# Kernel tuning notes

Measured on AMD Instinct MI355X. Metric: run time of the kernel, lower is better.

Reference implementation:

```python
import jax, jax.numpy as jnp
import numpy as np
import math

B, T, D = 1, 2048, 2048
H, HD = 16, 128          # n_head, head_dim = D // H
L = 512                  # latent_dims
RD = 64                  # rope_dims
K = 32                   # top-k selected tokens per query
THETA = 10000.0


def rope_tables(rd, t_max):
    freqs = 1.0 / (THETA ** (jnp.arange(0, rd, 2, dtype=jnp.float32) / rd))
    t = jnp.arange(t_max, dtype=jnp.float32)
    ang = jnp.outer(t, freqs)                      # (T, rd/2)
    cos = jnp.concatenate([jnp.cos(ang), jnp.cos(ang)], axis=-1)  # (T, rd)
    sin = jnp.concatenate([jnp.sin(ang), jnp.sin(ang)], axis=-1)
    return cos, sin


def rotate_half(x):
    d = x.shape[-1] // 2
    return jnp.concatenate([-x[..., d:], x[..., :d]], axis=-1)


def apply_rope(x, cos, sin):
    # x: (B, H, T, rd); cos/sin: (T, rd) -> broadcast over B, H
    t = x.shape[2]
    return x * cos[None, None, :t] + rotate_half(x) * sin[None, None, :t]


def setup_inputs() -> dict:
    key = jax.random.key(0)
    ks = jax.random.split(key, 10)
    s = lambda fan_in: 1.0 / math.sqrt(fan_in)
    inp = {
        'x': jax.random.normal(ks[0], (B, T, D), dtype=jnp.float32),
        'Wqd': jax.random.normal(ks[1], (D, L), dtype=jnp.float32) * s(D),
        'Wqu': jax.random.normal(ks[2], (L, D), dtype=jnp.float32) * s(L),
        'Wqr': jax.random.normal(ks[3], (L, H * RD), dtype=jnp.float32) * s(L),
        'Wkvd': jax.random.normal(ks[4], (D, L), dtype=jnp.float32) * s(D),
        'Wku': jax.random.normal(ks[5], (L, D), dtype=jnp.float32) * s(L),
        'Wvu': jax.random.normal(ks[6], (L, D), dtype=jnp.float32) * s(L),
        'Wkr': jax.random.normal(ks[7], (D, RD), dtype=jnp.float32) * s(D),
        'Wo': jax.random.normal(ks[8], (D, D), dtype=jnp.float32) * s(D),
        'topk_idx': jax.random.randint(ks[9], (B, T, K), 0, T, dtype=jnp.int64)
            if jax.config.jax_enable_x64 else
            jax.random.randint(ks[9], (B, T, K), 0, T, dtype=jnp.int32),
    }
    return inp


def reference(x, Wqd, Wqu, Wqr, Wkvd, Wku, Wvu, Wkr, Wo, topk_idx):
    cos, sin = rope_tables(RD, T)

    ql = x @ Wqd                                               # (B,T,L)
    q = (ql @ Wqu).reshape(B, T, H, HD).transpose(0, 2, 1, 3)  # (B,H,T,hd)
    qr = (ql @ Wqr).reshape(B, T, H, RD).transpose(0, 2, 1, 3)
    qr = apply_rope(qr, cos, sin)                              # (B,H,T,rd)

    ckv = x @ Wkvd                                             # (B,T,L)
    k = (ckv @ Wku).reshape(B, T, H, HD).transpose(0, 2, 1, 3) # (B,H,T,hd)
    v = (ckv @ Wvu).reshape(B, T, H, HD).transpose(0, 2, 1, 3)
    kr = apply_rope((x @ Wkr)[:, None], cos, sin)[:, 0]        # (B,T,rd) shared across heads

    # top-k gather sparse attention path
    flat = topk_idx.reshape(B, T * K)                          # (B, T*K)
    k_sel = jax.vmap(lambda a, i: a[:, i])(k, flat).reshape(B, H, T, K, HD)
    v_sel = jax.vmap(lambda a, i: a[:, i])(v, flat).reshape(B, H, T, K, HD)
    kr_sel = jax.vmap(lambda a, i: a[i])(kr, flat).reshape(B, T, K, RD)

    scale = 1.0 / math.sqrt(HD + RD)
    scores = (jnp.einsum('bhtd,bhtkd->bhtk', q, k_sel)
              + jnp.einsum('bhtd,btkd->bhtk', qr, kr_sel)) * scale
    attn = jax.nn.softmax(scores, axis=-1)                     # (B,H,T,K)
    out = jnp.einsum('bhtk,bhtkd->bhtd', attn, v_sel)          # (B,H,T,hd)
    out = out.transpose(0, 2, 1, 3).reshape(B, T, D)
    return out @ Wo
```

## Files before the change

kernel.cpp:

```cpp
#include <hip/hip_runtime.h>
#include <hip/hip_bf16.h>
#include <math.h>

typedef __hip_bfloat16 bf16;
typedef __attribute__((ext_vector_type(4))) float f32x4;
typedef __attribute__((ext_vector_type(8))) short s16x8;

#define T_SEQ 2048
#define DIM   2048
#define NH    16
#define LAT   512
#define RD    64
#define TOPK  32

typedef const __attribute__((address_space(1))) void* gas_ptr;
typedef __attribute__((address_space(3))) void* las_ptr;

struct GGroup {
    const bf16* A; const bf16* BT; bf16* C;
    int K, lda, ldb, ldc;
    int tx, ty, nz;
    long aZ, bZ, cZ;
    int tiles;
    int flags, N, t0;
};
struct GPack { GGroup g[4]; int n; };

template<int MT>
__global__ __launch_bounds__(256)
void gemm_group(GPack gp)
{
    constexpr int MI = MT / 64;
    constexpr int L  = 2 * MI + 2;

    int b = blockIdx.x;
    int gi = 0;
    while (gi < gp.n - 1 && b >= gp.g[gi].tiles) { b -= gp.g[gi].tiles; ++gi; }
    const GGroup g = gp.g[gi];

    const int per_z = g.tx * g.ty;
    const int z   = b / per_z;
    const int rem = b - z * per_z;
    const int bx  = rem % g.tx;
    const int by  = rem / g.tx;

    const bf16* A  = g.A  + (size_t)z * g.aZ;
    const bf16* BT = g.BT + (size_t)z * g.bZ;
    bf16*       C  = g.C  + (size_t)z * g.cZ;

    __shared__ bf16 aL[3][MT * 64];
    __shared__ bf16 bL[3][64 * 64];

    const int tid  = threadIdx.x;
    const int wave = tid >> 6;
    const int lane = tid & 63;
    const int quad = lane >> 4;
    const int l16  = lane & 15;

    const int tile_m = by * MT;
    const int tile_n = bx * 64;
    const int wrow = wave * (MT / 4);

    const int lrow = lane >> 3;
    const int lke  = (((lane & 7) ^ lrow) * 8);
    const int sw   = l16 & 15 & 7;

    f32x4 acc[MI][4] = {};

    const int nt = g.K >> 6;

    auto stage = [&](int t, int sb) {
        const int k0 = t << 6;
#pragma unroll
        for (int p = 0; p < 2 * MI; ++p) {
            const int R = (wave * 2 * MI + p) * 8;
            const bf16* src = A + (size_t)(tile_m + R + lrow) * g.lda + k0 + lke;
            __builtin_amdgcn_global_load_lds((gas_ptr)src, (las_ptr)(aL[sb] + R * 64), 16, 0, 0);
        }
#pragma unroll
        for (int p = 0; p < 2; ++p) {
            const int R = (wave * 2 + p) * 8;
            const bf16* src = BT + (size_t)(tile_n + R + lrow) * g.ldb + k0 + lke;
            __builtin_amdgcn_global_load_lds((gas_ptr)src, (las_ptr)(bL[sb] + R * 64), 16, 0, 0);
        }
    };

    stage(0, 0);
    if (nt > 1) stage(1, 1);

    int s = 0;
    for (int t = 0; t < nt; ++t) {
        if (t + 2 < nt) {
            int sn = s + 2; if (sn >= 3) sn -= 3;
            stage(t + 2, sn);
            asm volatile("s_waitcnt vmcnt(%0)" :: "n"(2 * L) : "memory");
        } else if (t + 1 < nt) {
            asm volatile("s_waitcnt vmcnt(%0)" :: "n"(L) : "memory");
        } else {
            asm volatile("s_waitcnt vmcnt(0)" ::: "memory");
        }
        __builtin_amdgcn_s_barrier();
        asm volatile("" ::: "memory");

#pragma unroll
        for (int ks = 0; ks < 2; ++ks) {
            s16x8 af[MI], bfr[4];
#pragma unroll
            for (int i = 0; i < MI; ++i)
                af[i] = *(const s16x8*)(&aL[s][(wrow + i * 16 + l16) * 64 +
                                               (((ks * 4 + quad) ^ sw) * 8)]);
#pragma unroll
            for (int j = 0; j < 4; ++j)
                bfr[j] = *(const s16x8*)(&bL[s][(j * 16 + l16) * 64 +
                                                (((ks * 4 + quad) ^ sw) * 8)]);

#pragma unroll
            for (int i = 0; i < MI; ++i)
#pragma unroll
                for (int j = 0; j < 4; ++j)
                    acc[i][j] = __builtin_amdgcn_mfma_f32_16x16x32_bf16(
                        af[i], bfr[j], acc[i][j], 0, 0, 0);
        }
        asm volatile("" ::: "memory");
        __builtin_amdgcn_s_barrier();
        ++s; if (s >= 3) s = 0;
    }

    if (g.flags & 1) {
#pragma unroll
        for (int jp = 0; jp < 2; ++jp) {
            const int colL = tile_n + jp * 16 + l16;
            if ((g.flags & 2) && colL >= g.N) continue;
            const float fr = powf(10000.f, -(float)(jp * 16 + l16) / 32.f);
#pragma unroll
            for (int i = 0; i < MI; ++i) {
#pragma unroll
                for (int r = 0; r < 4; ++r) {
                    const int row = tile_m + wrow + i * 16 + quad * 4 + r;
                    float sv, cv;
                    sincosf((float)(g.t0 + row) * fr, &sv, &cv);
                    const float x0 = acc[i][jp][r];
                    const float x1 = acc[i][jp + 2][r];
                    C[(size_t)row * g.ldc + colL]      = __float2bfloat16(x0 * cv - x1 * sv);
                    C[(size_t)row * g.ldc + colL + 32] = __float2bfloat16(x1 * cv + x0 * sv);
                }
            }
        }
    } else if (g.flags & 4) {
        float* Cf = (float*)C;
#pragma unroll
        for (int j = 0; j < 4; ++j) {
            const int col = tile_n + j * 16 + l16;
#pragma unroll
            for (int i = 0; i < MI; ++i)
#pragma unroll
                for (int r = 0; r < 4; ++r) {
                    const int row = tile_m + wrow + i * 16 + quad * 4 + r;
                    Cf[(size_t)row * g.ldc + col] = acc[i][j][r];
                }
        }
    } else {
#pragma unroll
        for (int j = 0; j < 4; ++j) {
            const int col = tile_n + j * 16 + l16;
            if ((g.flags & 2) && col >= g.N) continue;
#pragma unroll
            for (int i = 0; i < MI; ++i)
#pragma unroll
                for (int r = 0; r < 4; ++r) {
                    const int row = tile_m + wrow + i * 16 + quad * 4 + r;
                    C[(size_t)row * g.ldc + col] = __float2bfloat16(acc[i][j][r]);
                }
        }
    }
}

struct TDesc { const float* src; bf16* dst; int R; int C; int tiles; int ctiles; };
struct TPack { TDesc d[8]; int n; };

__global__ __launch_bounds__(256)
void transpose_batch(TPack p)
{
    int b = blockIdx.x;
    int mi = 0;
    while (mi < p.n - 1 && b >= p.d[mi].tiles) { b -= p.d[mi].tiles; ++mi; }
    const TDesc d = p.d[mi];
    const int tr = b / d.ctiles, tc = b % d.ctiles;
    const int r0 = tr * 32, c0 = tc * 32;

    __shared__ float lds[32][33];
    const int tx = threadIdx.x & 31, ty = threadIdx.x >> 5;
#pragma unroll
    for (int i = 0; i < 4; ++i)
        lds[ty * 4 + i][tx] = d.src[(size_t)(r0 + ty * 4 + i) * d.C + c0 + tx];
    __syncthreads();
#pragma unroll
    for (int i = 0; i < 4; ++i)
        d.dst[(size_t)(c0 + ty * 4 + i) * d.R + r0 + tx] =
            __float2bfloat16(lds[tx][ty * 4 + i]);
}

__global__ __launch_bounds__(256)
void convert2(const float* s0, bf16* d0, int n0,
              const float* s1, bf16* d1, int n1)
{
    int i = blockIdx.x * blockDim.x + threadIdx.x;
    const float* s; bf16* d;
    if (i < n0) { s = s0; d = d0; }
    else if (i < n0 + n1) { i -= n0; s = s1; d = d1; }
    else return;
    const float4 a = *(const float4*)(s + (size_t)i * 8);
    const float4 b = *(const float4*)(s + (size_t)i * 8 + 4);
    bf16 t[8];
    t[0] = __float2bfloat16(a.x); t[1] = __float2bfloat16(a.y);
    t[2] = __float2bfloat16(a.z); t[3] = __float2bfloat16(a.w);
    t[4] = __float2bfloat16(b.x); t[5] = __float2bfloat16(b.y);
    t[6] = __float2bfloat16(b.z); t[7] = __float2bfloat16(b.w);
    *(uint4*)(d + (size_t)i * 8) = *(uint4*)t;
}

__global__ __launch_bounds__(256)
void attn_mla(const bf16* __restrict__ qt,
              const bf16* __restrict__ qr,
              const bf16* __restrict__ xw,
              const bf16* __restrict__ kr,
              const int*  __restrict__ topk,
              bf16* __restrict__ U,
              int t0)
{
    __shared__ short ckv_s[32 * 520];
    __shared__ short qt_s[16 * 520];
    __shared__ short kr_s[32 * 72];
    __shared__ short qr_s[16 * 72];
    __shared__ short P_s[4][16 * 40];
    __shared__ int   idx_s[32];

    const int tl   = blockIdx.x;
    const int tg   = t0 + tl;
    const int tid  = threadIdx.x;
    const int wv   = tid >> 6;
    const int lane = tid & 63;
    const int quad = lane >> 4;
    const int l16  = lane & 15;

    if (tid < 32) {
        int j = topk[(size_t)tg * TOPK + tid];
        idx_s[tid] = (j < 0 || j >= T_SEQ) ? 0 : j;
    }
    __syncthreads();

#pragma unroll
    for (int i = 0; i < 8; ++i) {
        const int row = wv * 8 + i;
        const int j = idx_s[row];
        __builtin_amdgcn_global_load_lds(
            (gas_ptr)(xw + (size_t)j * 1024 + 512 + lane * 8),
            (las_ptr)(ckv_s + row * 520), 16, 0, 0);
    }
#pragma unroll
    for (int i = 0; i < 4; ++i) {
        const int seg = wv * 4 + i;
        __builtin_amdgcn_global_load_lds(
            (gas_ptr)(qt + (size_t)tl * 8192 + seg * 512 + lane * 8),
            (las_ptr)(qt_s + seg * 520), 16, 0, 0);
    }
    {
        const int row = tid >> 3, seg = tid & 7;
        const int j = idx_s[row];
        *(uint4*)(kr_s + row * 72 + seg * 8) =
            *(const uint4*)(kr + (size_t)j * RD + seg * 8);
    }
    if (tid < 128) {
        const int head = tid >> 3, seg = tid & 7;
        *(uint4*)(qr_s + head * 72 + seg * 8) =
            *(const uint4*)(qr + (size_t)tl * 1024 + head * 64 + seg * 8);
    }
    __syncthreads();

    f32x4 sc[2] = {};
#pragma unroll
    for (int ks = 0; ks < 16; ++ks) {
        s16x8 a  = *(const s16x8*)(qt_s + l16 * 520 + ks * 32 + quad * 8);
        s16x8 b0 = *(const s16x8*)(ckv_s + l16 * 520 + ks * 32 + quad * 8);
        s16x8 b1 = *(const s16x8*)(ckv_s + (16 + l16) * 520 + ks * 32 + quad * 8);
        sc[0] = __builtin_amdgcn_mfma_f32_16x16x32_bf16(a, b0, sc[0], 0, 0, 0);
        sc[1] = __builtin_amdgcn_mfma_f32_16x16x32_bf16(a, b1, sc[1], 0, 0, 0);
    }
#pragma unroll
    for (int ks = 0; ks < 2; ++ks) {
        s16x8 a  = *(const s16x8*)(qr_s + l16 * 72 + ks * 32 + quad * 8);
        s16x8 b0 = *(const s16x8*)(kr_s + l16 * 72 + ks * 32 + quad * 8);
        s16x8 b1 = *(const s16x8*)(kr_s + (16 + l16) * 72 + ks * 32 + quad * 8);
        sc[0] = __builtin_amdgcn_mfma_f32_16x16x32_bf16(a, b0, sc[0], 0, 0, 0);
        sc[1] = __builtin_amdgcn_mfma_f32_16x16x32_bf16(a, b1, sc[1], 0, 0, 0);
    }

    const float scale = 0.0721687836487032f;
    float inv[4];
    short* pw = P_s[wv];
#pragma unroll
    for (int r = 0; r < 4; ++r) {
        float s0 = sc[0][r] * scale, s1 = sc[1][r] * scale;
        float mx = fmaxf(s0, s1);
#pragma unroll
        for (int off = 1; off < 16; off <<= 1) mx = fmaxf(mx, __shfl_xor(mx, off));
        float p0 = __expf(s0 - mx), p1 = __expf(s1 - mx);
        float l = p0 + p1;
#pragma unroll
        for (int off = 1; off < 16; off <<= 1) l += __shfl_xor(l, off);
        inv[r] = 1.f / l;
        pw[(quad * 4 + r) * 40 + l16]      = __builtin_bit_cast(short, __float2bfloat16(p0));
        pw[(quad * 4 + r) * 40 + 16 + l16] = __builtin_bit_cast(short, __float2bfloat16(p1));
    }

    s16x8 ap = *(const s16x8*)(pw + l16 * 40 + quad * 8);
#pragma unroll
    for (int tt = 0; tt < 8; ++tt) {
        const int n0 = wv * 128 + tt * 16;
        s16x8 b;
#pragma unroll
        for (int j = 0; j < 8; ++j)
            b[j] = ckv_s[(quad * 8 + j) * 520 + n0 + l16];
        f32x4 u = {};
        u = __builtin_amdgcn_mfma_f32_16x16x32_bf16(ap, b, u, 0, 0, 0);
#pragma unroll
        for (int r = 0; r < 4; ++r)
            U[(size_t)tl * 8192 + (quad * 4 + r) * 512 + n0 + l16] =
                __float2bfloat16(u[r] * inv[r]);
    }
}

extern "C" void kernel_launch(void* const* d_in, const int* in_sizes, int n_in,
                              void* d_out, int out_size, void* d_ws, size_t ws_size,
                              hipStream_t stream)
{
    const float* x    = (const float*)d_in[0];
    const float* Wqd  = (const float*)d_in[1];
    const float* Wqu  = (const float*)d_in[2];
    const float* Wqr  = (const float*)d_in[3];
    const float* Wkvd = (const float*)d_in[4];
    const float* Wku  = (const float*)d_in[5];
    const float* Wvu  = (const float*)d_in[6];
    const float* Wkr  = (const float*)d_in[7];
    const float* Wo   = (const float*)d_in[8];
    const int*   topk = (const int*)d_in[9];
    float* out = (float*)d_out;

    const size_t KB = 1024;
    char* ws = (char*)d_ws;
    const bool flat = ws_size >= (size_t)128000 * KB;
    const int  TCH  = flat ? 2048 : 512;
    const int  NCH  = T_SEQ / TCH;

    size_t oXB, oWxT, oWkrT, oWquT, oWkub, oWqrT, oWvuT, oQ, oXW, oKR,
           oQR, oO, oWoT, oQT, oU;
    if (flat) {
        oXB = 0;       oWxT = 8192;   oWkrT = 12288; oWquT = 12544;
        oWkub = 14592; oWqrT = 16640; oWvuT = 17664; oQ = 19712;
        oXW = 27904;   oKR = 32000;   oQR = 32256;   oO = 36352;
        oWoT = 44544;  oQT = 52736;   oU = 85504;
    } else {
        oXW = 0;       oKR = 4096;    oWquT = 4352;  oWkub = 6400;
        oWqrT = 8448;  oWvuT = 9472;  oO = 11520;    oXB = 19712;
        oWxT = 27904;  oWkrT = 32000; oQ = 19712;    oQT = 21760;
        oQR = 29952;   oU = 30976;    oWoT = 21760;
    }
    bf16* xb   = (bf16*)(ws + oXB * KB);
    bf16* WxT  = (bf16*)(ws + oWxT * KB);
    bf16* WkrT = (bf16*)(ws + oWkrT * KB);
    bf16* WquT = (bf16*)(ws + oWquT * KB);
    bf16* Wkub = (bf16*)(ws + oWkub * KB);
    bf16* WqrT = (bf16*)(ws + oWqrT * KB);
    bf16* WvuT = (bf16*)(ws + oWvuT * KB);
    bf16* qB   = (bf16*)(ws + oQ * KB);
    bf16* xw   = (bf16*)(ws + oXW * KB);
    bf16* kr   = (bf16*)(ws + oKR * KB);
    bf16* qrC  = (bf16*)(ws + oQR * KB);
    bf16* o    = (bf16*)(ws + oO * KB);
    bf16* WoT  = (bf16*)(ws + oWoT * KB);
    bf16* qtC  = (bf16*)(ws + oQT * KB);
    bf16* uC   = (bf16*)(ws + oU * KB);

    dim3 blk(256);

    {
        int n0 = T_SEQ * DIM / 8, n1 = LAT * DIM / 8;
        convert2<<<(n0 + n1 + 255) / 256, blk, 0, stream>>>(x, xb, n0, Wku, Wkub, n1);
        TPack p;
        p.d[0] = { Wqd,  WxT,                   DIM, LAT,  (DIM/32)*(LAT/32),  LAT/32 };
        p.d[1] = { Wkvd, WxT + (size_t)LAT*DIM, DIM, LAT,  (DIM/32)*(LAT/32),  LAT/32 };
        p.d[2] = { Wkr,  WkrT,                  DIM, RD,   (DIM/32)*(RD/32),   RD/32  };
        p.d[3] = { Wqr,  WqrT,                  LAT, 1024, (LAT/32)*(1024/32), 1024/32 };
        p.d[4] = { Wvu,  WvuT,                  LAT, DIM,  (LAT/32)*(DIM/32),  DIM/32 };
        p.d[5] = { Wqu,  WquT,                  LAT, DIM,  (LAT/32)*(DIM/32),  DIM/32 };
        p.n = 6;
        int tot = 0;
        for (int i = 0; i < p.n; ++i) tot += p.d[i].tiles;
        if (flat) {
            p.d[6] = { Wo, WoT, DIM, DIM, (DIM/32)*(DIM/32), DIM/32 };
            p.n = 7; tot += p.d[6].tiles;
        }
        transpose_batch<<<tot, blk, 0, stream>>>(p);
    }

    {
        GPack gp;
        gp.g[0] = { xb, WxT,  xw, DIM, DIM, DIM, 1024, 1024/64, T_SEQ/64, 1,
                    0, 0, 0, (1024/64)*(T_SEQ/64), 0, 1024, 0 };
        gp.g[1] = { xb, WkrT, kr, DIM, DIM, DIM, RD,   1,       T_SEQ/64, 1,
                    0, 0, 0, T_SEQ/64, 1 , RD, 0 };
        gp.n = 2;
        gemm_group<64><<<gp.g[0].tiles + gp.g[1].tiles, blk, 0, stream>>>(gp);
    }

    for (int c = 0; c < NCH; ++c) {
        const int t0 = c * TCH;
        bf16* q  = flat ? qB  + (size_t)t0 * 2048 : qB;
        bf16* qt = flat ? qtC + (size_t)t0 * 8192 : qtC;
        bf16* qr = flat ? qrC + (size_t)t0 * 1024 : qrC;
        bf16* U  = flat ? uC  + (size_t)t0 * 8192 : uC;
        const bf16* xwc = xw + (size_t)t0 * 1024;

        {
            GPack gp;
            gp.g[0] = { xwc, WquT, q,  LAT, 1024, LAT, 2048, 2048/64, TCH/128, 1,
                        0, 0, 0, (2048/64)*(TCH/128), 0, 2048, 0 };
            gp.g[1] = { xwc, WqrT, qr, LAT, 1024, LAT, 1024, 1024/64, TCH/128, 1,
                        0, 0, 0, (1024/64)*(TCH/128), 1 , 1024, t0 };
            gp.n = 2;
            gemm_group<128><<<gp.g[0].tiles + gp.g[1].tiles, blk, 0, stream>>>(gp);
        }
        {
            GPack gp;
            gp.g[0] = { q, Wkub, qt, 128, 2048, 2048, 8192, 512/64, TCH/128, NH,
                        128, 128, 512, (512/64)*(TCH/128)*NH, 0, 512, 0 };
            gp.n = 1;
            gemm_group<128><<<gp.g[0].tiles, blk, 0, stream>>>(gp);
        }
        attn_mla<<<TCH, blk, 0, stream>>>(qt, qr, xw, kr, topk, U, t0);
        {
            GPack gp;
            gp.g[0] = { U, WvuT, o + (size_t)t0 * DIM, LAT, 8192, LAT, DIM,
                        2, TCH/128, NH, 512, (long)128*LAT, 128,
                        2*(TCH/128)*NH, 0, 128, 0 };
            gp.n = 1;
            gemm_group<128><<<gp.g[0].tiles, blk, 0, stream>>>(gp);
        }
    }

    if (!flat) {
        TPack p;
        p.d[0] = { Wo, WoT, DIM, DIM, (DIM/32)*(DIM/32), DIM/32 };
        p.n = 1;
        transpose_batch<<<p.d[0].tiles, blk, 0, stream>>>(p);
    }
    {
        GPack gp;
        gp.g[0] = { o, WoT, (bf16*)out, DIM, DIM, DIM, DIM,
                    DIM/64, T_SEQ/128, 1, 0, 0, 0,
                    (DIM/64)*(T_SEQ/128), 4 , DIM, 0 };
        gp.n = 1;
        gemm_group<128><<<gp.g[0].tiles, blk, 0, stream>>>(gp);
    }
}
```

Baseline: 250.8 us.

## Switch GEMM to double buffering, split-K output projection with atomics, larger tiles

The GEMM kernel drops from a three-stage LDS ring to two buffers, issuing the next tile's load before computing on the current one and waiting with a full vmcnt(0) plus a barrier at the end of each iteration. This lowers LDS use per block, which may raise occupancy, but it gives up one stage of prefetch depth. The output projection now splits K into two halves that accumulate into the fp32 output with atomic adds, which requires a new zero-fill kernel up front, so it gains parallelism at the cost of atomic traffic. The down-projection GEMM moves from 64-row to 128-row tiles.

```diff
diff --git a/kernel.cpp b/kernel.cpp
--- a/kernel.cpp
+++ b/kernel.cpp
@@ -31,7 +31,6 @@
 void gemm_group(GPack gp)
 {
     constexpr int MI = MT / 64;
-    constexpr int L  = 2 * MI + 2;
 
     int b = blockIdx.x;
     int gi = 0;
@@ -48,8 +47,8 @@
     const bf16* BT = g.BT + (size_t)z * g.bZ;
     bf16*       C  = g.C  + (size_t)z * g.cZ;
 
-    __shared__ bf16 aL[3][MT * 64];
-    __shared__ bf16 bL[3][64 * 64];
+    __shared__ bf16 aL[2][MT * 64];
+    __shared__ bf16 bL[2][64 * 64];
 
     const int tid  = threadIdx.x;
     const int wave = tid >> 6;
@@ -63,7 +62,7 @@
 
     const int lrow = lane >> 3;
     const int lke  = (((lane & 7) ^ lrow) * 8);
-    const int sw   = l16 & 15 & 7;
+    const int sw   = l16 & 7;
 
     f32x4 acc[MI][4] = {};
 
@@ -86,33 +85,24 @@
     };
 
     stage(0, 0);
-    if (nt > 1) stage(1, 1);
-
-    int s = 0;
+    asm volatile("s_waitcnt vmcnt(0)" ::: "memory");
+    __builtin_amdgcn_s_barrier();
+
+    int cur = 0;
     for (int t = 0; t < nt; ++t) {
-        if (t + 2 < nt) {
-            int sn = s + 2; if (sn >= 3) sn -= 3;
-            stage(t + 2, sn);
-            asm volatile("s_waitcnt vmcnt(%0)" :: "n"(2 * L) : "memory");
-        } else if (t + 1 < nt) {
-            asm volatile("s_waitcnt vmcnt(%0)" :: "n"(L) : "memory");
-        } else {
-            asm volatile("s_waitcnt vmcnt(0)" ::: "memory");
-        }
-        __builtin_amdgcn_s_barrier();
-        asm volatile("" ::: "memory");
+        if (t + 1 < nt) stage(t + 1, cur ^ 1);
 
 #pragma unroll
         for (int ks = 0; ks < 2; ++ks) {
             s16x8 af[MI], bfr[4];
 #pragma unroll
             for (int i = 0; i < MI; ++i)
-                af[i] = *(const s16x8*)(&aL[s][(wrow + i * 16 + l16) * 64 +
-                                               (((ks * 4 + quad) ^ sw) * 8)]);
+                af[i] = *(const s16x8*)(&aL[cur][(wrow + i * 16 + l16) * 64 +
+                                                 (((ks * 4 + quad) ^ sw) * 8)]);
 #pragma unroll
             for (int j = 0; j < 4; ++j)
-                bfr[j] = *(const s16x8*)(&bL[s][(j * 16 + l16) * 64 +
-                                                (((ks * 4 + quad) ^ sw) * 8)]);
+                bfr[j] = *(const s16x8*)(&bL[cur][(j * 16 + l16) * 64 +
+                                                  (((ks * 4 + quad) ^ sw) * 8)]);
 
 #pragma unroll
             for (int i = 0; i < MI; ++i)
@@ -121,9 +111,10 @@
                     acc[i][j] = __builtin_amdgcn_mfma_f32_16x16x32_bf16(
                         af[i], bfr[j], acc[i][j], 0, 0, 0);
         }
-        asm volatile("" ::: "memory");
+
+        asm volatile("s_waitcnt vmcnt(0)" ::: "memory");
         __builtin_amdgcn_s_barrier();
-        ++s; if (s >= 3) s = 0;
+        cur ^= 1;
     }
 
     if (g.flags & 1) {
@@ -157,6 +148,19 @@
                 for (int r = 0; r < 4; ++r) {
                     const int row = tile_m + wrow + i * 16 + quad * 4 + r;
                     Cf[(size_t)row * g.ldc + col] = acc[i][j][r];
+                }
+        }
+    } else if (g.flags & 8) {
+        float* Cf = (float*)C;
+#pragma unroll
+        for (int j = 0; j < 4; ++j) {
+            const int col = tile_n + j * 16 + l16;
+#pragma unroll
+            for (int i = 0; i < MI; ++i)
+#pragma unroll
+                for (int r = 0; r < 4; ++r) {
+                    const int row = tile_m + wrow + i * 16 + quad * 4 + r;
+                    unsafeAtomicAdd(&Cf[(size_t)row * g.ldc + col], acc[i][j][r]);
                 }
         }
     } else {
@@ -217,6 +221,16 @@
     t[4] = __float2bfloat16(b.x); t[5] = __float2bfloat16(b.y);
     t[6] = __float2bfloat16(b.z); t[7] = __float2bfloat16(b.w);
     *(uint4*)(d + (size_t)i * 8) = *(uint4*)t;
+}
+
+__global__ __launch_bounds__(256)
+void zero_f32(float* p, int n4)
+{
+    int i = blockIdx.x * blockDim.x + threadIdx.x;
+    if (i < n4) {
+        float4 z = {0.f, 0.f, 0.f, 0.f};
+        ((float4*)p)[i] = z;
+    }
 }
 
 __global__ __launch_bounds__(256)
@@ -384,6 +398,7 @@
     dim3 blk(256);
 
     {
+        zero_f32<<<(T_SEQ * DIM / 4 + 255) / 256, blk, 0, stream>>>(out, T_SEQ * DIM / 4);
         int n0 = T_SEQ * DIM / 8, n1 = LAT * DIM / 8;
         convert2<<<(n0 + n1 + 255) / 256, blk, 0, stream>>>(x, xb, n0, Wku, Wkub, n1);
         TPack p;
@@ -405,12 +420,12 @@
 
     {
         GPack gp;
-        gp.g[0] = { xb, WxT,  xw, DIM, DIM, DIM, 1024, 1024/64, T_SEQ/64, 1,
-                    0, 0, 0, (1024/64)*(T_SEQ/64), 0, 1024, 0 };
-        gp.g[1] = { xb, WkrT, kr, DIM, DIM, DIM, RD,   1,       T_SEQ/64, 1,
-                    0, 0, 0, T_SEQ/64, 1 , RD, 0 };
+        gp.g[0] = { xb, WxT,  xw, DIM, DIM, DIM, 1024, 1024/64, T_SEQ/128, 1,
+                    0, 0, 0, (1024/64)*(T_SEQ/128), 0, 1024, 0 };
+        gp.g[1] = { xb, WkrT, kr, DIM, DIM, DIM, RD,   1,       T_SEQ/128, 1,
+                    0, 0, 0, T_SEQ/128, 1 , RD, 0 };
         gp.n = 2;
-        gemm_group<64><<<gp.g[0].tiles + gp.g[1].tiles, blk, 0, stream>>>(gp);
+        gemm_group<128><<<gp.g[0].tiles + gp.g[1].tiles, blk, 0, stream>>>(gp);
     }
 
     for (int c = 0; c < NCH; ++c) {
@@ -456,9 +471,9 @@
     }
     {
         GPack gp;
-        gp.g[0] = { o, WoT, (bf16*)out, DIM, DIM, DIM, DIM,
-                    DIM/64, T_SEQ/128, 1, 0, 0, 0,
-                    (DIM/64)*(T_SEQ/128), 4 , DIM, 0 };
+        gp.g[0] = { o, WoT, (bf16*)out, 1024, DIM, DIM, DIM,
+                    DIM/64, T_SEQ/128, 2, 1024, 1024, 0,
+                    (DIM/64)*(T_SEQ/128)*2, 8 , DIM, 0 };
         gp.n = 1;
         gemm_group<128><<<gp.g[0].tiles, blk, 0, stream>>>(gp);
     }
```

New measurement: 281.1 us. +12.1%, slower.
